# Kernel tuning notes

Measured on AMD Instinct MI355X. Metric: run time of the kernel, lower is better.

Reference implementation:

```python
import jax, jax.numpy as jnp
import numpy as np

OUT, IN = 11008, 4096  # out_features, in_features (IN even, 64-aligned -> no pad columns)
B, S = 4, 2048


def setup_inputs() -> dict:
    key = jax.random.key(0)
    k1, k2, k3, k4 = jax.random.split(key, 4)
    x = jax.random.normal(k1, (B, S, IN), dtype=jnp.float32)
    # packed int4: each byte holds two unsigned nibbles in [0, 15] (q + 7), low_first order
    packed = jax.random.randint(k2, (OUT, IN // 2), 0, 256, dtype=jnp.int32)
    # per-output-channel scale = max_abs / 7; small positive values
    scale = jax.random.uniform(k3, (OUT,), dtype=jnp.float32, minval=1e-4, maxval=0.02)
    bias = jax.random.normal(k4, (OUT,), dtype=jnp.float32)
    return {"x": x, "packed": packed, "scale": scale, "bias": bias}


def _dequant(packed, scale):
    # low_first nibble order: q0 = low nibble, q1 = high nibble
    q0 = packed & 15
    q1 = (packed >> 4) & 15
    # interleave: columns [q0_0, q1_0, q0_1, q1_1, ...] -> (OUT, IN)
    q_u = jnp.stack([q0, q1], axis=-1).reshape(packed.shape[0], -1)
    q = q_u[:, :IN] - 7  # symmetric int4 values in [-7, 7]
    return q.astype(jnp.float32) * scale[:, None]  # (OUT, IN)


def reference(x, packed, scale, bias):
    w = _dequant(packed, scale)  # (OUT, IN) fp32
    # y = x @ w.T + bias
    return jnp.einsum('bsi,oi->bso', x, w) + bias
```

## Files before the change

### kernel.cpp

```cpp
#include <hip/hip_runtime.h>
#include <hip/hip_bf16.h>

#define MM 8192
#define NN 11008
#define KK 4096
#define PKW 2048

#define BM 256
#define BN 256
#define BKI 128
#define NTI (KK / BKI)
#define NBM (MM / BM)
#define NBN (NN / BN)

typedef __attribute__((ext_vector_type(4)))  float f32x4;
typedef __attribute__((ext_vector_type(4)))  int   i32x4;
typedef __attribute__((ext_vector_type(16))) int   i32x16;
typedef __attribute__((ext_vector_type(8)))  short s16x8;
typedef __attribute__((ext_vector_type(4)))  short s16x4;

typedef __attribute__((address_space(3))) unsigned char        lds_u8;
typedef const __attribute__((address_space(1))) unsigned char  glb_u8;

static __device__ __forceinline__ unsigned short f2bf(float f) {
  union { float f; unsigned int u; } v; v.f = f;
  unsigned int u = v.u;
  u += 0x7fffu + ((u >> 16) & 1u);
  return (unsigned short)(u >> 16);
}



__global__ __launch_bounds__(256) void int4lin_quant_x(
    const float* __restrict__ X, signed char* __restrict__ O, float* __restrict__ xs)
{
  const int row  = blockIdx.x;
  const int t    = threadIdx.x;
  const int lane = t & 63;
  const int wave = t >> 6;
  const float* xr = X + (size_t)row * KK;

  f32x4 v[4];
  float mx = 0.0f;
#pragma unroll
  for (int j = 0; j < 4; ++j) {
    v[j] = *(const f32x4*)(xr + t * 16 + j * 4);
#pragma unroll
    for (int e = 0; e < 4; ++e) mx = fmaxf(mx, fabsf(v[j][e]));
  }
#pragma unroll
  for (int off = 32; off; off >>= 1) mx = fmaxf(mx, __shfl_xor(mx, off));
  __shared__ float red[4];
  if (lane == 0) red[wave] = mx;
  __syncthreads();
  mx = fmaxf(fmaxf(red[0], red[1]), fmaxf(red[2], red[3]));
  mx = fmaxf(mx, 1e-30f);
  const float rs = 127.0f / mx;
  if (t == 0) xs[row] = mx / 127.0f;

  i32x4 o;
#pragma unroll
  for (int w = 0; w < 4; ++w) {
    int acc = 0;
#pragma unroll
    for (int e = 0; e < 4; ++e) {
      int q = __float2int_rn(v[w][e] * rs);
      q = max(-127, min(127, q));
      acc |= (q & 0xff) << (8 * e);
    }
    o[w] = acc;
  }
  signed char* dst = O + (size_t)(row >> 8) * 1048576
                       + (size_t)(t >> 3) * 32768 + (size_t)(t & 7) * 4096
                       + (size_t)(row & 255) * 16;
  *(i32x4*)dst = o;
}


__global__ void int4lin_quant_w(const int* __restrict__ P, signed char* __restrict__ O) {
  const int ntot = NN * 256;
  int i = blockIdx.x * blockDim.x + threadIdx.x;
  const int stride = gridDim.x * blockDim.x;
  for (; i < ntot; i += stride) {
    const int row = i >> 8;
    const int gr  = i & 255;
    const int* src = P + (size_t)row * PKW + gr * 8;
    i32x4 va = *(const i32x4*)src;
    i32x4 vb = *(const i32x4*)(src + 4);
    i32x4 o;
#pragma unroll
    for (int h = 0; h < 2; ++h) {
      i32x4 w = h ? vb : va;
#pragma unroll
      for (int p = 0; p < 2; ++p) {
        const int b0 = w[2 * p], b1 = w[2 * p + 1];
        const int q0 = (b0 & 15) - 7, q1 = ((b0 >> 4) & 15) - 7;
        const int q2 = (b1 & 15) - 7, q3 = ((b1 >> 4) & 15) - 7;
        o[h * 2 + p] = (q0 & 0xff) | ((q1 & 0xff) << 8) | ((q2 & 0xff) << 16) | ((q3 & 0xff) << 24);
      }
    }
    signed char* dst = O + (size_t)(row >> 8) * 1048576
                         + (size_t)(gr >> 3) * 32768 + (size_t)(gr & 7) * 4096
                         + (size_t)(row & 255) * 16;
    *(i32x4*)dst = o;
  }
}


__global__ __launch_bounds__(512, 2) void int4lin_gemm_i8(
    const signed char* __restrict__ Ai,
    const signed char* __restrict__ Bi,
    const float* __restrict__ xs,
    const float* __restrict__ scale,
    const float* __restrict__ bias,
    float* __restrict__ C)
{
  __shared__ signed char As[2][32768];
  __shared__ signed char Bs[2][32768];

  const int tid  = threadIdx.x;
  const int lane = tid & 63;
  const int wave = tid >> 6;
  const int wm = wave >> 2;
  const int wn = wave & 3;

  const int bid = blockIdx.x;
  const int swz = (bid & 7) * 172 + (bid >> 3);
  const int bm = swz / NBN;
  const int bn = swz - bm * NBN;

  const signed char* Abase = Ai + (size_t)bm * 1048576;
  const signed char* Bbase = Bi + (size_t)bn * 1048576;

  const int r5   = lane & 31;
  const int half = lane >> 5;

  i32x16 acc[4][2] = {};

  const int aoff0 = half * 4096 + (wm * 128 + r5) * 16;
  const int boff0 = half * 4096 + (wn * 64 + r5) * 16;

#define LDA(buf, mf, ks) (*(const i32x4*)(&As[buf][aoff0 + (ks) * 8192 + (mf) * 512]))
#define LDB(buf, nf, ks) (*(const i32x4*)(&Bs[buf][boff0 + (ks) * 8192 + (nf) * 512]))

  auto stage = [&](int buf, int kb) {
    const glb_u8* as = (const glb_u8*)(Abase + (size_t)kb * 32768 + tid * 16);
    const glb_u8* bs = (const glb_u8*)(Bbase + (size_t)kb * 32768 + tid * 16);
#pragma unroll
    for (int g = 0; g < 4; ++g)
      __builtin_amdgcn_global_load_lds(as + g * 8192,
          (lds_u8*)(&As[buf][g * 8192 + tid * 16]), 16, 0, 0);
#pragma unroll
    for (int g = 0; g < 4; ++g)
      __builtin_amdgcn_global_load_lds(bs + g * 8192,
          (lds_u8*)(&Bs[buf][g * 8192 + tid * 16]), 16, 0, 0);
  };

  stage(0, 0);
  asm volatile("s_waitcnt vmcnt(0)\n\ts_barrier" ::: "memory");

#pragma unroll 1
  for (int t = 0; t < NTI; ++t) {
    const int buf = t & 1;

    if (t + 1 < NTI) stage(buf ^ 1, t + 1);

#pragma unroll
    for (int ks = 0; ks < 4; ++ks) {
      i32x4 a[4], b[2];
#pragma unroll
      for (int mf = 0; mf < 4; ++mf) a[mf] = LDA(buf, mf, ks);
#pragma unroll
      for (int nf = 0; nf < 2; ++nf) b[nf] = LDB(buf, nf, ks);
      __builtin_amdgcn_s_setprio(1);
#pragma unroll
      for (int mf = 0; mf < 4; ++mf) {
        acc[mf][0] = __builtin_amdgcn_mfma_i32_32x32x32_i8(a[mf], b[0], acc[mf][0], 0, 0, 0);
        acc[mf][1] = __builtin_amdgcn_mfma_i32_32x32x32_i8(a[mf], b[1], acc[mf][1], 0, 0, 0);
      }
      __builtin_amdgcn_s_setprio(0);
    }

    if (t + 1 < NTI)
      asm volatile("s_waitcnt vmcnt(0)\n\ts_barrier" ::: "memory");
  }

  const size_t m0 = (size_t)bm * BM;
  const int colb = bn * BN + wn * 64 + r5;
#pragma unroll
  for (int mf = 0; mf < 4; ++mf) {
    const size_t rbase = m0 + wm * 128 + mf * 32 + 4 * half;
#pragma unroll
    for (int reg = 0; reg < 16; ++reg) {
      const size_t row = rbase + (reg & 3) + 8 * (reg >> 2);
      const float xsr = xs[row];
      float* cp = C + row * NN + colb;
#pragma unroll
      for (int nf = 0; nf < 2; ++nf) {
        const int col = colb + nf * 32;
        __builtin_nontemporal_store(
            (float)acc[mf][nf][reg] * xsr * scale[col] + bias[col], cp + nf * 32);
      }
    }
  }
#undef LDA
#undef LDB
}


__global__ __launch_bounds__(256) void int4lin_gemm_inline(
    const float* __restrict__ X,
    const int* __restrict__ P,
    const float* __restrict__ scale,
    const float* __restrict__ bias,
    float* __restrict__ C)
{
  __shared__ unsigned short As[128 * 64];
  __shared__ unsigned short Bs[128 * 64];

  const int tid  = threadIdx.x;
  const int lane = tid & 63;
  const int wave = tid >> 6;
  const int m0 = blockIdx.y * 128;
  const int n0 = blockIdx.x * 128;
  const int wr = (wave >> 1) * 64;
  const int wc = (wave & 1) * 64;

  f32x4 acc[4][4] = {};

  for (int kt = 0; kt < KK; kt += 64) {
#pragma unroll
    for (int i = 0; i < 8; ++i) {
      const int idx = i * 256 + tid;
      const int row = idx >> 4;
      const int c   = (idx & 15) << 2;
      f32x4 v = *(const f32x4*)(X + (size_t)(m0 + row) * KK + kt + c);
      s16x4 o;
      o[0] = (short)f2bf(v[0]); o[1] = (short)f2bf(v[1]);
      o[2] = (short)f2bf(v[2]); o[3] = (short)f2bf(v[3]);
      *(s16x4*)(As + row * 64 + (c ^ ((row & 7) << 3))) = o;
    }
#pragma unroll
    for (int i = 0; i < 4; ++i) {
      const int idx = i * 256 + tid;
      const int row = idx >> 3;
      const int c   = (idx & 7) << 3;
      i32x4 v = *(const i32x4*)(P + (size_t)(n0 + row) * PKW + ((kt + c) >> 1));
      s16x8 o;
#pragma unroll
      for (int j = 0; j < 4; ++j) {
        const int b = v[j];
        o[2 * j]     = (short)f2bf((float)((b & 15) - 7));
        o[2 * j + 1] = (short)f2bf((float)(((b >> 4) & 15) - 7));
      }
      *(s16x8*)(Bs + row * 64 + (c ^ ((row & 7) << 3))) = o;
    }
    __syncthreads();
#pragma unroll
    for (int kk = 0; kk < 2; ++kk) {
      const int rsel = lane & 15;
      const int ksel = ((((lane >> 4) << 3) + kk * 32)) ^ ((lane & 7) << 3);
      s16x8 af[4], bfr[4];
#pragma unroll
      for (int m = 0; m < 4; ++m)
        af[m] = *(const s16x8*)(As + (wr + m * 16 + rsel) * 64 + ksel);
#pragma unroll
      for (int n = 0; n < 4; ++n)
        bfr[n] = *(const s16x8*)(Bs + (wc + n * 16 + rsel) * 64 + ksel);
#pragma unroll
      for (int m = 0; m < 4; ++m)
#pragma unroll
        for (int n = 0; n < 4; ++n)
          acc[m][n] = __builtin_amdgcn_mfma_f32_16x16x32_bf16(af[m], bfr[n], acc[m][n], 0, 0, 0);
    }
    __syncthreads();
  }

  const int crow = wr + ((lane >> 4) << 2);
  const int ccol = wc + (lane & 15);
#pragma unroll
  for (int n = 0; n < 4; ++n) {
    const int gc = n0 + ccol + n * 16;
    const float sc = scale[gc];
    const float bi = bias[gc];
#pragma unroll
    for (int m = 0; m < 4; ++m) {
      float* cp = C + (size_t)(m0 + crow + m * 16) * NN + gc;
#pragma unroll
      for (int r = 0; r < 4; ++r)
        cp[(size_t)r * NN] = acc[m][n][r] * sc + bi;
    }
  }
}


extern "C" void kernel_launch(void* const* d_in, const int* in_sizes, int n_in,
                              void* d_out, int out_size, void* d_ws, size_t ws_size,
                              hipStream_t stream) {
  const float* x      = (const float*)d_in[0];
  const int*   packed = (const int*)d_in[1];
  const float* scale  = (const float*)d_in[2];
  const float* bias   = (const float*)d_in[3];
  float* y = (float*)d_out;

  const size_t nXA = (size_t)MM * KK;
  const size_t nWB = (size_t)NN * KK;
  const size_t nXS = (size_t)MM * sizeof(float);
  if (ws_size >= nXA + nWB + nXS) {
    signed char* xi = (signed char*)d_ws;
    signed char* wi = (signed char*)d_ws + nXA;
    float*       xsv = (float*)((char*)d_ws + nXA + nWB);
    int4lin_quant_x<<<MM, 256, 0, stream>>>(x, xi, xsv);
    int4lin_quant_w<<<2048, 256, 0, stream>>>(packed, wi);
    int4lin_gemm_i8<<<NBM * NBN, 512, 0, stream>>>(xi, wi, xsv, scale, bias, y);
    return;
  }
  dim3 grid(NN / 128, MM / 128);
  int4lin_gemm_inline<<<grid, 256, 0, stream>>>(x, packed, scale, bias, y);
}
```

Baseline: 540.9 us.

## Load B operand directly from global into registers, drop B LDS staging

The B tile is no longer staged through shared memory. Each wave loads its own B fragments straight from global memory into registers, double-buffered across k-tiles with manual ping-pong unrolling, while A keeps the LDS async path. This halves LDS traffic and footprint and removes the LDS reads for B. In exchange it adds register pressure (16 extra i32x4 per lane), and B reuse across the wm waves now goes through L1/L2 rather than LDS. The full vmcnt(0) wait per tile may also expose latency.

```diff
diff --git a/kernel.cpp b/kernel.cpp
--- a/kernel.cpp
+++ b/kernel.cpp
@@ -116,7 +116,6 @@
     float* __restrict__ C)
 {
   __shared__ signed char As[2][32768];
-  __shared__ signed char Bs[2][32768];
 
   const int tid  = threadIdx.x;
   const int lane = tid & 63;
@@ -138,51 +137,59 @@
   i32x16 acc[4][2] = {};
 
   const int aoff0 = half * 4096 + (wm * 128 + r5) * 16;
-  const int boff0 = half * 4096 + (wn * 64 + r5) * 16;
+  const int blane = half * 4096 + (wn * 64 + r5) * 16;
 
 #define LDA(buf, mf, ks) (*(const i32x4*)(&As[buf][aoff0 + (ks) * 8192 + (mf) * 512]))
-#define LDB(buf, nf, ks) (*(const i32x4*)(&Bs[buf][boff0 + (ks) * 8192 + (nf) * 512]))
-
-  auto stage = [&](int buf, int kb) {
+
+  auto stageA = [&](int buf, int kb) {
     const glb_u8* as = (const glb_u8*)(Abase + (size_t)kb * 32768 + tid * 16);
-    const glb_u8* bs = (const glb_u8*)(Bbase + (size_t)kb * 32768 + tid * 16);
 #pragma unroll
     for (int g = 0; g < 4; ++g)
       __builtin_amdgcn_global_load_lds(as + g * 8192,
           (lds_u8*)(&As[buf][g * 8192 + tid * 16]), 16, 0, 0);
-#pragma unroll
-    for (int g = 0; g < 4; ++g)
-      __builtin_amdgcn_global_load_lds(bs + g * 8192,
-          (lds_u8*)(&Bs[buf][g * 8192 + tid * 16]), 16, 0, 0);
   };
 
-  stage(0, 0);
-  asm volatile("s_waitcnt vmcnt(0)\n\ts_barrier" ::: "memory");
-
-#pragma unroll 1
-  for (int t = 0; t < NTI; ++t) {
-    const int buf = t & 1;
-
-    if (t + 1 < NTI) stage(buf ^ 1, t + 1);
-
+  auto loadB = [&](int kb, i32x4 (&br)[4][2]) {
+    const signed char* p = Bbase + (size_t)kb * 32768 + blane;
+#pragma unroll
+    for (int ks = 0; ks < 4; ++ks)
+#pragma unroll
+      for (int nf = 0; nf < 2; ++nf)
+        br[ks][nf] = *(const i32x4*)(p + ks * 8192 + nf * 512);
+  };
+
+  i32x4 b0[4][2], b1[4][2];
+
+  auto tile = [&](int t, int buf, i32x4 (&bc)[4][2], i32x4 (&bn_)[4][2]) {
+    if (t + 1 < NTI) {
+      stageA(buf ^ 1, t + 1);
+      loadB(t + 1, bn_);
+    }
 #pragma unroll
     for (int ks = 0; ks < 4; ++ks) {
-      i32x4 a[4], b[2];
+      i32x4 a[4];
 #pragma unroll
       for (int mf = 0; mf < 4; ++mf) a[mf] = LDA(buf, mf, ks);
-#pragma unroll
-      for (int nf = 0; nf < 2; ++nf) b[nf] = LDB(buf, nf, ks);
       __builtin_amdgcn_s_setprio(1);
 #pragma unroll
       for (int mf = 0; mf < 4; ++mf) {
-        acc[mf][0] = __builtin_amdgcn_mfma_i32_32x32x32_i8(a[mf], b[0], acc[mf][0], 0, 0, 0);
-        acc[mf][1] = __builtin_amdgcn_mfma_i32_32x32x32_i8(a[mf], b[1], acc[mf][1], 0, 0, 0);
+        acc[mf][0] = __builtin_amdgcn_mfma_i32_32x32x32_i8(a[mf], bc[ks][0], acc[mf][0], 0, 0, 0);
+        acc[mf][1] = __builtin_amdgcn_mfma_i32_32x32x32_i8(a[mf], bc[ks][1], acc[mf][1], 0, 0, 0);
       }
       __builtin_amdgcn_s_setprio(0);
     }
-
     if (t + 1 < NTI)
       asm volatile("s_waitcnt vmcnt(0)\n\ts_barrier" ::: "memory");
+  };
+
+  stageA(0, 0);
+  loadB(0, b0);
+  asm volatile("s_waitcnt vmcnt(8)\n\ts_barrier" ::: "memory");
+
+#pragma unroll 1
+  for (int tt = 0; tt < NTI; tt += 2) {
+    tile(tt,     0, b0, b1);
+    tile(tt + 1, 1, b1, b0);
   }
 
   const size_t m0 = (size_t)bm * BM;
@@ -204,7 +211,6 @@
     }
   }
 #undef LDA
-#undef LDB
 }
 
 
```

New measurement: 540.2 us. No clear change (-0.1%).

## Load int8 GEMM fragments directly from global into registers, dropping LDS staging

Applied to the files above, without the earlier changes.

Removes the LDS double buffers and the async global-to-LDS staging with barriers. Each wave now loads its own MFMA fragments straight from global memory into registers, with a two-step register ping-pong so one step's loads overlap the other step's MFMAs. This removes LDS traffic and block-wide barriers. In exchange, each wave fetches its tiles separately, so data previously shared across the waves of a block is re-read through L2/L1, and global load latency is hidden only one step ahead.

```diff
diff --git a/kernel.cpp b/kernel.cpp
--- a/kernel.cpp
+++ b/kernel.cpp
@@ -10,6 +10,7 @@
 #define BN 256
 #define BKI 128
 #define NTI (KK / BKI)
+#define NSTEP (NTI * 4)
 #define NBM (MM / BM)
 #define NBN (NN / BN)
 
@@ -115,9 +116,6 @@
     const float* __restrict__ bias,
     float* __restrict__ C)
 {
-  __shared__ signed char As[2][32768];
-  __shared__ signed char Bs[2][32768];
-
   const int tid  = threadIdx.x;
   const int lane = tid & 63;
   const int wave = tid >> 6;
@@ -129,60 +127,43 @@
   const int bm = swz / NBN;
   const int bn = swz - bm * NBN;
 
-  const signed char* Abase = Ai + (size_t)bm * 1048576;
-  const signed char* Bbase = Bi + (size_t)bn * 1048576;
-
   const int r5   = lane & 31;
   const int half = lane >> 5;
 
+  const signed char* pA = Ai + (size_t)bm * 1048576 + half * 4096
+                             + (wm * 128 + r5) * 16;
+  const signed char* pB = Bi + (size_t)bn * 1048576 + half * 4096
+                             + (wn * 64 + r5) * 16;
+
   i32x16 acc[4][2] = {};
 
-  const int aoff0 = half * 4096 + (wm * 128 + r5) * 16;
-  const int boff0 = half * 4096 + (wn * 64 + r5) * 16;
-
-#define LDA(buf, mf, ks) (*(const i32x4*)(&As[buf][aoff0 + (ks) * 8192 + (mf) * 512]))
-#define LDB(buf, nf, ks) (*(const i32x4*)(&Bs[buf][boff0 + (ks) * 8192 + (nf) * 512]))
-
-  auto stage = [&](int buf, int kb) {
-    const glb_u8* as = (const glb_u8*)(Abase + (size_t)kb * 32768 + tid * 16);
-    const glb_u8* bs = (const glb_u8*)(Bbase + (size_t)kb * 32768 + tid * 16);
-#pragma unroll
-    for (int g = 0; g < 4; ++g)
-      __builtin_amdgcn_global_load_lds(as + g * 8192,
-          (lds_u8*)(&As[buf][g * 8192 + tid * 16]), 16, 0, 0);
-#pragma unroll
-    for (int g = 0; g < 4; ++g)
-      __builtin_amdgcn_global_load_lds(bs + g * 8192,
-          (lds_u8*)(&Bs[buf][g * 8192 + tid * 16]), 16, 0, 0);
+  auto loadf = [&](int s, i32x4 (&ar)[4], i32x4 (&br)[2]) {
+    const size_t off = (size_t)s * 8192;
+#pragma unroll
+    for (int mf = 0; mf < 4; ++mf) ar[mf] = *(const i32x4*)(pA + off + mf * 512);
+#pragma unroll
+    for (int nf = 0; nf < 2; ++nf) br[nf] = *(const i32x4*)(pB + off + nf * 512);
   };
 
-  stage(0, 0);
-  asm volatile("s_waitcnt vmcnt(0)\n\ts_barrier" ::: "memory");
+#define SWEEP(aR, bR)                                                                       \
+  __builtin_amdgcn_s_setprio(1);                                                            \
+  _Pragma("unroll")                                                                         \
+  for (int mf = 0; mf < 4; ++mf) {                                                          \
+    acc[mf][0] = __builtin_amdgcn_mfma_i32_32x32x32_i8(aR[mf], bR[0], acc[mf][0], 0, 0, 0); \
+    acc[mf][1] = __builtin_amdgcn_mfma_i32_32x32x32_i8(aR[mf], bR[1], acc[mf][1], 0, 0, 0); \
+  }                                                                                         \
+  __builtin_amdgcn_s_setprio(0);
+
+  i32x4 aE[4], bE[2], aO[4], bO[2];
+
+  loadf(0, aE, bE);
 
 #pragma unroll 1
-  for (int t = 0; t < NTI; ++t) {
-    const int buf = t & 1;
-
-    if (t + 1 < NTI) stage(buf ^ 1, t + 1);
-
-#pragma unroll
-    for (int ks = 0; ks < 4; ++ks) {
-      i32x4 a[4], b[2];
-#pragma unroll
-      for (int mf = 0; mf < 4; ++mf) a[mf] = LDA(buf, mf, ks);
-#pragma unroll
-      for (int nf = 0; nf < 2; ++nf) b[nf] = LDB(buf, nf, ks);
-      __builtin_amdgcn_s_setprio(1);
-#pragma unroll
-      for (int mf = 0; mf < 4; ++mf) {
-        acc[mf][0] = __builtin_amdgcn_mfma_i32_32x32x32_i8(a[mf], b[0], acc[mf][0], 0, 0, 0);
-        acc[mf][1] = __builtin_amdgcn_mfma_i32_32x32x32_i8(a[mf], b[1], acc[mf][1], 0, 0, 0);
-      }
-      __builtin_amdgcn_s_setprio(0);
-    }
-
-    if (t + 1 < NTI)
-      asm volatile("s_waitcnt vmcnt(0)\n\ts_barrier" ::: "memory");
+  for (int s = 0; s < NSTEP; s += 2) {
+    loadf(s + 1, aO, bO);
+    SWEEP(aE, bE)
+    loadf((s + 2 < NSTEP) ? s + 2 : NSTEP - 1, aE, bE);
+    SWEEP(aO, bO)
   }
 
   const size_t m0 = (size_t)bm * BM;
@@ -203,8 +184,7 @@
       }
     }
   }
-#undef LDA
-#undef LDB
+#undef SWEEP
 }
 
 
```

Result: slower. 592.6 us (+9.6%).
